# Kernel optimization log

Hardware: AMD Instinct MI355X
Metric: run time of the kernel (lower is better)

## Reference

```python
import jax, jax.numpy as jnp
import numpy as np

L, B = 128, 4
N_D, N_E, N_PROJ, DEPTH = 1024, 256, 256, 4
N_V = 128000
CUTOFFS = (10000, 20000, 40000, 60000, 100000)  # hard-coded in Model.__init__
N_CLUSTERS = len(CUTOFFS)
HIGHWAY_BIAS = -3.0  # args.bias, added to forget-gate bias
EMB_SCALE = float(np.sqrt(N_D))


def setup_inputs() -> dict:
    key = jax.random.key(0)
    ks = jax.random.split(key, 10)
    s = 0.02
    return {
        "x": jax.random.randint(ks[0], (L, B), 0, N_V),
        "y": jax.random.randint(ks[1], (L, B), 0, N_V),
        "hidden": jnp.zeros((DEPTH, B, N_D), jnp.float32),
        "emb_weight": jax.random.normal(ks[2], (N_V, N_E), jnp.float32) * s,
        "emb_proj": jax.random.normal(ks[3], (N_D, N_E), jnp.float32) * s,
        "out_bias": jnp.zeros((N_V,), jnp.float32),
        "cluster_weight": jax.random.normal(ks[4], (N_CLUSTERS, N_E), jnp.float32) * s,
        "cluster_bias": jnp.zeros((N_CLUSTERS,), jnp.float32),
        "Wp": jax.random.normal(ks[5], (DEPTH, N_D, N_PROJ), jnp.float32) * s,
        "Wq": jax.random.normal(ks[6], (DEPTH, N_PROJ, 3 * N_D), jnp.float32) * s,
        "wc": jax.random.normal(ks[7], (DEPTH, 2 * N_D), jnp.float32) * s,
        "b": jnp.zeros((DEPTH, 2 * N_D), jnp.float32),
    }


def _sru_layer(h, c0, Wp_l, Wq_l, wc_l, b_l):
    # Projected linear: [L,B,n_d] @ [n_d,n_proj] @ [n_proj,3*n_d]
    u = ((h @ Wp_l) @ Wq_l).reshape(L, B, 3, N_D)
    u0, u1, u2 = u[..., 0, :], u[..., 1, :], u[..., 2, :]
    vf, vr = wc_l[:N_D], wc_l[N_D:]
    bf = b_l[:N_D] + HIGHWAY_BIAS
    br = b_l[N_D:]

    def step(c, uu):
        u0t, u1t, u2t, xt = uu
        f = jax.nn.sigmoid(u1t + vf * c + bf)
        r = jax.nn.sigmoid(u2t + vr * c + br)
        c_new = f * c + (1.0 - f) * u0t
        h_t = r * c_new + (1.0 - r) * xt  # highway connection (rescale off)
        return c_new, h_t

    c_last, hs = jax.lax.scan(step, c0, (u0, u1, u2, h))
    return hs, c_last


def reference(x, y, hidden, emb_weight, emb_proj, out_bias, cluster_weight,
              cluster_bias, Wp, Wq, wc, b):
    # Adaptive embedding (div_val=1: single table + projection), scaled by sqrt(n_d)
    h = (emb_weight[x] @ emb_proj.T) * EMB_SCALE  # [L,B,n_d]
    c_finals = []
    for l in range(DEPTH):
        h, cl = _sru_layer(h, hidden[l], Wp[l], Wq[l], wc[l], b[l])
        c_finals.append(cl)
    hid_out = jnp.stack(c_finals)  # [depth,B,n_d]

    out = h.reshape(-1, N_D)       # [N, n_d]
    proj_h = out @ emb_proj        # tied out_proj: [N, n_e]
    c0 = CUTOFFS[0]

    # Head: first cutoff tokens + cluster logits
    head_w = jnp.concatenate([emb_weight[:c0], cluster_weight], axis=0)
    head_b = jnp.concatenate([out_bias[:c0], cluster_bias], axis=0)
    head_lp = jax.nn.log_softmax(proj_h @ head_w.T + head_b, axis=-1)  # [N, c0+5]

    # Tail logits over all tail tokens; per-cluster logsumexp via static slices
    tail_logits = proj_h @ emb_weight[c0:].T + out_bias[c0:]  # [N, N_V-c0]
    bounds = list(CUTOFFS) + [N_V]
    lses = jnp.stack(
        [jax.scipy.special.logsumexp(tail_logits[:, bounds[i] - c0:bounds[i + 1] - c0], axis=-1)
         for i in range(N_CLUSTERS)], axis=-1)  # [N, 5]

    yf = y.reshape(-1)
    cluster = jnp.zeros_like(yf)
    for cu in CUTOFFS:
        cluster = cluster + (yf >= cu).astype(yf.dtype)  # 0=head, 1..5=tails
    n_idx = jnp.arange(yf.shape[0])
    logit_y = jnp.sum(proj_h * emb_weight[yf], axis=-1) + out_bias[yf]
    tci = jnp.clip(cluster - 1, 0, N_CLUSTERS - 1)
    tail_lp_y = logit_y - lses[n_idx, tci]
    head_tok_lp = head_lp[n_idx, jnp.minimum(yf, c0 - 1)]
    cluster_lp = head_lp[n_idx, c0 + tci]
    lp = jnp.where(cluster == 0, head_tok_lp, cluster_lp + tail_lp_y)
    loss = (-lp).reshape(L, B)
    return loss, hid_out
```

## Files before the change

kernel.cpp:

```cpp
#include <hip/hip_runtime.h>
#include <hip/hip_bf16.h>
#include <math.h>

#define LSEQ 128
#define BB 4
#define NTOK 512
#define ND 1024
#define NE 256
#define NPROJ 256
#define DEPTH 4
#define NV 128000
#define NC 5
#define C0 10000
#define NHEADROWS 128005
#define NROWS_PAD 128128

typedef unsigned short u16;
typedef __bf16 bf16x8 __attribute__((ext_vector_type(8)));
typedef float  f32x4  __attribute__((ext_vector_type(4)));
typedef u16    u16x8  __attribute__((ext_vector_type(8)));
typedef u16    u16x4  __attribute__((ext_vector_type(4)));

__device__ inline u16 f2bf_rne(float f) {
  unsigned int u = __float_as_uint(f);
  u += 0x7FFFu + ((u >> 16) & 1u);
  return (u16)(u >> 16);
}
__device__ inline unsigned int f2hilo_pk(float v) {
  unsigned int u = __float_as_uint(v);
  u16 h = (u16)(u >> 16);
  u16 l = f2bf_rne(v - __uint_as_float(u & 0xFFFF0000u));
  return (unsigned int)h | ((unsigned int)l << 16);
}

__global__ __launch_bounds__(256) void conv_emb(
    const float* __restrict__ emb, const float* __restrict__ cw,
    u16* __restrict__ Wb) {
  const long NCH = (long)NHEADROWS * NE / 8;
  const long EMBN = (long)NV * NE;
  for (long i = (long)blockIdx.x * 256 + threadIdx.x; i < NCH; i += (long)gridDim.x * 256) {
    long e = i * 8;
    const float* src = (e < EMBN) ? emb + e : cw + (e - EMBN);
    float4 a = *reinterpret_cast<const float4*>(src);
    float4 b = *reinterpret_cast<const float4*>(src + 4);
    u16x8 o;
    o[0] = f2bf_rne(a.x); o[1] = f2bf_rne(a.y); o[2] = f2bf_rne(a.z); o[3] = f2bf_rne(a.w);
    o[4] = f2bf_rne(b.x); o[5] = f2bf_rne(b.y); o[6] = f2bf_rne(b.z); o[7] = f2bf_rne(b.w);
    *reinterpret_cast<u16x8*>(Wb + e) = o;
  }
}

__global__ __launch_bounds__(256) void conv_hilo(
    const float* __restrict__ src, u16* __restrict__ dh, u16* __restrict__ dl, long n4) {
  for (long i = (long)blockIdx.x * 256 + threadIdx.x; i < n4; i += (long)gridDim.x * 256) {
    float4 a = *reinterpret_cast<const float4*>(src + i * 4);
    unsigned int p0 = f2hilo_pk(a.x), p1 = f2hilo_pk(a.y);
    unsigned int p2 = f2hilo_pk(a.z), p3 = f2hilo_pk(a.w);
    u16x4 h, l;
    h[0] = (u16)p0; l[0] = (u16)(p0 >> 16);
    h[1] = (u16)p1; l[1] = (u16)(p1 >> 16);
    h[2] = (u16)p2; l[2] = (u16)(p2 >> 16);
    h[3] = (u16)p3; l[3] = (u16)(p3 >> 16);
    *reinterpret_cast<u16x4*>(dh + i * 4) = h;
    *reinterpret_cast<u16x4*>(dl + i * 4) = l;
  }
}

__global__ __launch_bounds__(256) void tconv(
    const float* __restrict__ src, u16* __restrict__ dh, u16* __restrict__ dl,
    int K, int N, long sStride, long dStride) {
  __shared__ float t[32][33];
  const int mat = blockIdx.z;
  src += (long)mat * sStride; dh += (long)mat * dStride; dl += (long)mat * dStride;
  const int k0 = blockIdx.y * 32, n0 = blockIdx.x * 32;
  const int lr = threadIdx.x & 31, tr = threadIdx.x >> 5;
#pragma unroll
  for (int i = 0; i < 4; ++i)
    t[tr + i * 8][lr] = src[(size_t)(k0 + tr + i * 8) * N + n0 + lr];
  __syncthreads();
#pragma unroll
  for (int i = 0; i < 4; ++i) {
    int nl = tr + i * 8;
    unsigned int pk = f2hilo_pk(t[lr][nl]);
    size_t o = (size_t)(n0 + nl) * K + k0 + lr;
    dh[o] = (u16)pk; dl[o] = (u16)(pk >> 16);
  }
}

__global__ __launch_bounds__(256) void gather_hilo(
    const int* __restrict__ x, const float* __restrict__ emb,
    u16* __restrict__ Eh, u16* __restrict__ El) {
  int n = blockIdx.x, e = threadIdx.x;
  float v = emb[(size_t)x[n] * NE + e] * 32.0f;
  unsigned int pk = f2hilo_pk(v);
  Eh[(size_t)n * NE + e] = (u16)pk; El[(size_t)n * NE + e] = (u16)(pk >> 16);
}

#define GP 72
template<bool WF32, bool WHILO, bool WRNE>
__global__ __launch_bounds__(256) void gemm3(
    const u16* __restrict__ Ah, const u16* __restrict__ Al,
    const u16* __restrict__ Bh, const u16* __restrict__ Bl,
    float* __restrict__ C, u16* __restrict__ Ch, u16* __restrict__ Cl,
    u16* __restrict__ Cr, int M, int N, int K) {
  __shared__ u16 ash[64][GP], asl[64][GP], bsh[64][GP], bsl[64][GP];
  const int tid = threadIdx.x, lane = tid & 63, w = tid >> 6;
  const int wm = w >> 1, wn = w & 1, lrow = lane & 15, lkg = lane >> 4;
  const int m0 = blockIdx.y * 64, n0 = blockIdx.x * 64;
  f32x4 acc[2][2] = {};
  for (int ks = 0; ks < K; ks += 64) {
#pragma unroll
    for (int i = 0; i < 2; ++i) {
      int idx = tid + 256 * i, r = idx >> 3, c8 = (idx & 7) * 8;
      *reinterpret_cast<u16x8*>(&ash[r][c8]) = *reinterpret_cast<const u16x8*>(Ah + (size_t)(m0 + r) * K + ks + c8);
      *reinterpret_cast<u16x8*>(&asl[r][c8]) = *reinterpret_cast<const u16x8*>(Al + (size_t)(m0 + r) * K + ks + c8);
      *reinterpret_cast<u16x8*>(&bsh[r][c8]) = *reinterpret_cast<const u16x8*>(Bh + (size_t)(n0 + r) * K + ks + c8);
      *reinterpret_cast<u16x8*>(&bsl[r][c8]) = *reinterpret_cast<const u16x8*>(Bl + (size_t)(n0 + r) * K + ks + c8);
    }
    __syncthreads();
#pragma unroll
    for (int k2 = 0; k2 < 2; ++k2) {
      bf16x8 ah[2], al[2], bh[2], bl[2];
#pragma unroll
      for (int mi = 0; mi < 2; ++mi) {
        ah[mi] = *reinterpret_cast<const bf16x8*>(&ash[wm * 32 + mi * 16 + lrow][k2 * 32 + lkg * 8]);
        al[mi] = *reinterpret_cast<const bf16x8*>(&asl[wm * 32 + mi * 16 + lrow][k2 * 32 + lkg * 8]);
      }
#pragma unroll
      for (int ni = 0; ni < 2; ++ni) {
        bh[ni] = *reinterpret_cast<const bf16x8*>(&bsh[wn * 32 + ni * 16 + lrow][k2 * 32 + lkg * 8]);
        bl[ni] = *reinterpret_cast<const bf16x8*>(&bsl[wn * 32 + ni * 16 + lrow][k2 * 32 + lkg * 8]);
      }
#pragma unroll
      for (int mi = 0; mi < 2; ++mi)
#pragma unroll
        for (int ni = 0; ni < 2; ++ni) {
          acc[mi][ni] = __builtin_amdgcn_mfma_f32_16x16x32_bf16(ah[mi], bh[ni], acc[mi][ni], 0, 0, 0);
          acc[mi][ni] = __builtin_amdgcn_mfma_f32_16x16x32_bf16(ah[mi], bl[ni], acc[mi][ni], 0, 0, 0);
          acc[mi][ni] = __builtin_amdgcn_mfma_f32_16x16x32_bf16(al[mi], bh[ni], acc[mi][ni], 0, 0, 0);
        }
    }
    __syncthreads();
  }
#pragma unroll
  for (int mi = 0; mi < 2; ++mi)
#pragma unroll
    for (int ni = 0; ni < 2; ++ni)
#pragma unroll
      for (int j = 0; j < 4; ++j) {
        int row = m0 + wm * 32 + mi * 16 + lkg * 4 + j;
        int col = n0 + wn * 32 + ni * 16 + lrow;
        float v = acc[mi][ni][j];
        size_t o = (size_t)row * N + col;
        if (WF32) C[o] = v;
        if (WHILO) { unsigned int pk = f2hilo_pk(v); Ch[o] = (u16)pk; Cl[o] = (u16)(pk >> 16); }
        if (WRNE) Cr[o] = f2bf_rne(v);
      }
}

__global__ __launch_bounds__(256) void sru_scan(
    const float* __restrict__ u, const float* __restrict__ h_in,
    const float* __restrict__ hidden, const float* __restrict__ wcv,
    const float* __restrict__ bvec, float* __restrict__ h_out,
    u16* __restrict__ hOh, u16* __restrict__ hOl,
    float* __restrict__ out, int layer) {
  int idx = blockIdx.x * 256 + threadIdx.x;
  int b = idx >> 10, d = idx & 1023;
  float c = hidden[layer * (BB * ND) + idx];
  float vf = wcv[layer * 2 * ND + d];
  float vr = wcv[layer * 2 * ND + ND + d];
  float bf = bvec[layer * 2 * ND + d] + (-3.0f);
  float br = bvec[layer * 2 * ND + ND + d];
  for (int t0 = 0; t0 < LSEQ; t0 += 4) {
    float u0[4], u1[4], u2[4], xt[4];
#pragma unroll
    for (int q = 0; q < 4; ++q) {
      size_t row = (size_t)(t0 + q) * BB + b;
      u0[q] = u[row * (3 * ND) + d];
      u1[q] = u[row * (3 * ND) + ND + d];
      u2[q] = u[row * (3 * ND) + 2 * ND + d];
      xt[q] = h_in[row * ND + d];
    }
#pragma unroll
    for (int q = 0; q < 4; ++q) {
      float f = 1.f / (1.f + __expf(-(u1[q] + vf * c + bf)));
      float r = 1.f / (1.f + __expf(-(u2[q] + vr * c + br)));
      c = f * c + (1.f - f) * u0[q];
      float h = r * c + (1.f - r) * xt[q];
      size_t row = (size_t)(t0 + q) * BB + b;
      h_out[row * ND + d] = h;
      unsigned int pk = f2hilo_pk(h);
      hOh[row * ND + d] = (u16)pk; hOl[row * ND + d] = (u16)(pk >> 16);
    }
  }
  out[NTOK + layer * (BB * ND) + idx] = c;
}

__device__ inline int seg_of(int v) {
  if (v < 10000)  return 5;
  if (v < 20000)  return 0;
  if (v < 40000)  return 1;
  if (v < 60000)  return 2;
  if (v < 100000) return 3;
  if (v < 128000) return 4;
  if (v < 128005) return 5;
  return -1;
}

__global__ __launch_bounds__(256) void head_tail(
    const u16* __restrict__ Wb, const float* __restrict__ ob,
    const float* __restrict__ cb, const u16* __restrict__ phb,
    float* __restrict__ accum) {
  __shared__ u16 As[128][GP];
  __shared__ u16 Bs[128][GP];
  __shared__ float red[128][6];
  const int tid = threadIdx.x, lane = tid & 63, w = tid >> 6;
  const int wr = w >> 1, wcq = w & 1, lrow = lane & 15, lkg = lane >> 4;

  const int nwg = gridDim.x;
  const int orig = blockIdx.x;
  const int xcd = orig & 7, i8 = orig >> 3;
  const int q = nwg >> 3, r8 = nwg & 7;
  const int swz = (xcd < r8 ? xcd * (q + 1) : r8 * (q + 1) + (xcd - r8) * q) + i8;
  const int v0 = (swz >> 2) * 128;
  const int n0 = (swz & 3) * 128;

  f32x4 acc[4][4] = {};
  for (int ks = 0; ks < NE; ks += 64) {
#pragma unroll
    for (int i = 0; i < 4; ++i) {
      int idx = tid + 256 * i, rr = idx >> 3, c8 = (idx & 7) * 8;
      *reinterpret_cast<u16x8*>(&As[rr][c8]) =
          *reinterpret_cast<const u16x8*>(Wb + (size_t)(v0 + rr) * NE + ks + c8);
    }
#pragma unroll
    for (int i = 0; i < 4; ++i) {
      int idx = tid + 256 * i, rr = idx >> 3, c8 = (idx & 7) * 8;
      *reinterpret_cast<u16x8*>(&Bs[rr][c8]) =
          *reinterpret_cast<const u16x8*>(phb + (size_t)(n0 + rr) * NE + ks + c8);
    }
    __syncthreads();
#pragma unroll
    for (int k2 = 0; k2 < 2; ++k2) {
      bf16x8 av[4], bv[4];
#pragma unroll
      for (int mi = 0; mi < 4; ++mi)
        av[mi] = *reinterpret_cast<const bf16x8*>(&As[wr * 64 + mi * 16 + lrow][k2 * 32 + lkg * 8]);
#pragma unroll
      for (int ni = 0; ni < 4; ++ni)
        bv[ni] = *reinterpret_cast<const bf16x8*>(&Bs[wcq * 64 + ni * 16 + lrow][k2 * 32 + lkg * 8]);
#pragma unroll
      for (int mi = 0; mi < 4; ++mi)
#pragma unroll
        for (int ni = 0; ni < 4; ++ni)
          acc[mi][ni] = __builtin_amdgcn_mfma_f32_16x16x32_bf16(av[mi], bv[ni], acc[mi][ni], 0, 0, 0);
    }
    __syncthreads();
  }

  for (int i = tid; i < 128 * 6; i += 256) red[i / 6][i % 6] = 0.f;
  __syncthreads();
#pragma unroll
  for (int ni = 0; ni < 4; ++ni) {
    int tok = wcq * 64 + ni * 16 + lrow;
    float s[6] = {0.f, 0.f, 0.f, 0.f, 0.f, 0.f};
#pragma unroll
    for (int mi = 0; mi < 4; ++mi) {
#pragma unroll
      for (int j = 0; j < 4; ++j) {
        int v = v0 + wr * 64 + mi * 16 + lkg * 4 + j;
        int seg = seg_of(v);
        if (seg >= 0) {
          float bias = (v < NV) ? ob[v] : cb[v - NV];
          s[seg] += expf(acc[mi][ni][j] + bias);
        }
      }
    }
#pragma unroll
    for (int sg = 0; sg < 6; ++sg)
      if (s[sg] != 0.f) atomicAdd(&red[tok][sg], s[sg]);
  }
  __syncthreads();
  for (int i = tid; i < 128 * 6; i += 256) {
    float s = red[i / 6][i % 6];
    if (s != 0.f) atomicAdd(&accum[(size_t)(n0 + i / 6) * 6 + (i % 6)], s);
  }
}

__global__ __launch_bounds__(64) void loss_kernel(
    const float* __restrict__ ph, const float* __restrict__ emb,
    const float* __restrict__ cw, const float* __restrict__ ob,
    const float* __restrict__ cb, const int* __restrict__ y,
    const float* __restrict__ accum, float* __restrict__ out) {
  int n = blockIdx.x, lane = threadIdx.x;
  int yv = y[n];
  int cluster = (yv >= 10000) + (yv >= 20000) + (yv >= 40000) + (yv >= 60000) + (yv >= 100000);
  int tci = min(max(cluster - 1, 0), NC - 1);
  int hy = min(yv, C0 - 1);
  float d1 = 0.f, d2 = 0.f, d3 = 0.f;
  for (int k = lane; k < NE; k += 64) {
    float p = ph[(size_t)n * NE + k];
    d1 += p * emb[(size_t)yv * NE + k];
    d2 += p * emb[(size_t)hy * NE + k];
    d3 += p * cw[(size_t)tci * NE + k];
  }
#pragma unroll
  for (int off = 32; off > 0; off >>= 1) {
    d1 += __shfl_down(d1, off);
    d2 += __shfl_down(d2, off);
    d3 += __shfl_down(d3, off);
  }
  if (lane == 0) {
    float logit_y = d1 + ob[yv];
    float head_tok = d2 + ob[hy];
    float clus = d3 + cb[tci];
    float head_lse = logf(accum[(size_t)n * 6 + 5]);
    float lp;
    if (cluster == 0) lp = head_tok - head_lse;
    else lp = (clus - head_lse) + (logit_y - logf(accum[(size_t)n * 6 + tci]));
    out[n] = -lp;
  }
}

extern "C" void kernel_launch(void* const* d_in, const int* in_sizes, int n_in,
                              void* d_out, int out_size, void* d_ws, size_t ws_size,
                              hipStream_t stream) {
  const int*   x      = (const int*)d_in[0];
  const int*   y      = (const int*)d_in[1];
  const float* hidden = (const float*)d_in[2];
  const float* emb    = (const float*)d_in[3];
  const float* eproj  = (const float*)d_in[4];
  const float* obias  = (const float*)d_in[5];
  const float* cwp    = (const float*)d_in[6];
  const float* cbp    = (const float*)d_in[7];
  const float* Wp     = (const float*)d_in[8];
  const float* Wq     = (const float*)d_in[9];
  const float* wcv    = (const float*)d_in[10];
  const float* bvec   = (const float*)d_in[11];
  float* out = (float*)d_out;

  char* p = (char*)d_ws;
  auto alloc = [&](size_t bytes) { char* r = p; p += (bytes + 255) & ~(size_t)255; return r; };
  u16*   WbB   = (u16*)alloc((size_t)NROWS_PAD * NE * 2);
  u16*   epH   = (u16*)alloc((size_t)ND * NE * 2);
  u16*   epL   = (u16*)alloc((size_t)ND * NE * 2);
  u16*   epTH  = (u16*)alloc((size_t)NE * ND * 2);
  u16*   epTL  = (u16*)alloc((size_t)NE * ND * 2);
  u16*   WpTH  = (u16*)alloc((size_t)DEPTH * NPROJ * ND * 2);
  u16*   WpTL  = (u16*)alloc((size_t)DEPTH * NPROJ * ND * 2);
  u16*   WqTH  = (u16*)alloc((size_t)DEPTH * 3 * ND * NPROJ * 2);
  u16*   WqTL  = (u16*)alloc((size_t)DEPTH * 3 * ND * NPROJ * 2);
  u16*   ExH   = (u16*)alloc((size_t)NTOK * NE * 2);
  u16*   ExL   = (u16*)alloc((size_t)NTOK * NE * 2);
  float* h0    = (float*)alloc((size_t)NTOK * ND * 4);
  float* h1    = (float*)alloc((size_t)NTOK * ND * 4);
  u16*   h0H   = (u16*)alloc((size_t)NTOK * ND * 2);
  u16*   h0L   = (u16*)alloc((size_t)NTOK * ND * 2);
  u16*   h1H   = (u16*)alloc((size_t)NTOK * ND * 2);
  u16*   h1L   = (u16*)alloc((size_t)NTOK * ND * 2);
  u16*   PH    = (u16*)alloc((size_t)NTOK * NPROJ * 2);
  u16*   PL    = (u16*)alloc((size_t)NTOK * NPROJ * 2);
  float* U     = (float*)alloc((size_t)NTOK * 3 * ND * 4);
  float* projh = (float*)alloc((size_t)NTOK * NE * 4);
  u16*   phb   = (u16*)alloc((size_t)NTOK * NE * 2);
  float* accum = (float*)alloc((size_t)NTOK * 6 * 4);

  (void)hipMemsetAsync(accum, 0, (size_t)NTOK * 6 * 4, stream);

  conv_hilo<<<256, 256, 0, stream>>>(eproj, epH, epL, (long)ND * NE / 4);
  tconv<<<dim3(NE / 32, ND / 32, 1), 256, 0, stream>>>(eproj, epTH, epTL, ND, NE, 0, 0);
  tconv<<<dim3(NPROJ / 32, ND / 32, DEPTH), 256, 0, stream>>>(
      Wp, WpTH, WpTL, ND, NPROJ, (long)ND * NPROJ, (long)ND * NPROJ);
  tconv<<<dim3(3 * ND / 32, NPROJ / 32, DEPTH), 256, 0, stream>>>(
      Wq, WqTH, WqTL, NPROJ, 3 * ND, (long)NPROJ * 3 * ND, (long)NPROJ * 3 * ND);
  gather_hilo<<<NTOK, NE, 0, stream>>>(x, emb, ExH, ExL);

  gemm3<true, true, false><<<dim3(ND / 64, NTOK / 64), 256, 0, stream>>>(
      ExH, ExL, epH, epL, h0, h0H, h0L, nullptr, NTOK, ND, NE);

  float* hcF = h0; u16* hcH = h0H; u16* hcL = h0L;
  float* hnF = h1; u16* hnH = h1H; u16* hnL = h1L;
  for (int l = 0; l < DEPTH; ++l) {
    gemm3<false, true, false><<<dim3(NPROJ / 64, NTOK / 64), 256, 0, stream>>>(
        hcH, hcL, WpTH + (size_t)l * NPROJ * ND, WpTL + (size_t)l * NPROJ * ND,
        nullptr, PH, PL, nullptr, NTOK, NPROJ, ND);
    gemm3<true, false, false><<<dim3(3 * ND / 64, NTOK / 64), 256, 0, stream>>>(
        PH, PL, WqTH + (size_t)l * 3 * ND * NPROJ, WqTL + (size_t)l * 3 * ND * NPROJ,
        U, nullptr, nullptr, nullptr, NTOK, 3 * ND, NPROJ);
    sru_scan<<<16, 256, 0, stream>>>(U, hcF, hidden, wcv, bvec, hnF, hnH, hnL, out, l);
    { float* t = hcF; hcF = hnF; hnF = t; }
    { u16* t = hcH; hcH = hnH; hnH = t; }
    { u16* t = hcL; hcL = hnL; hnL = t; }
  }

  gemm3<true, false, true><<<dim3(NE / 64, NTOK / 64), 256, 0, stream>>>(
      hcH, hcL, epTH, epTL, projh, nullptr, nullptr, phb, NTOK, NE, ND);

  conv_emb<<<2048, 256, 0, stream>>>(emb, cwp, WbB);

  head_tail<<<dim3((NTOK / 128) * (NROWS_PAD / 128)), 256, 0, stream>>>(
      WbB, obias, cbp, phb, accum);

  loss_kernel<<<NTOK, 64, 0, stream>>>(projh, emb, cwp, obias, cbp, y, accum, out);
}
```

Before: 648.2 us.

## Double-buffer head GEMM with direct-to-LDS loads, swizzle, and prefetch SRU inputs

The head/tail logsumexp GEMM now stages tiles with global_load_lds into double-buffered, XOR-swizzled shared memory, so the next K slice loads while MFMAs run. LDS bank conflicts are reduced without the padding. Its epilogue hoists the segment lookup per 16-row group, uses __expf, and issues one atomic per group instead of six-way branching. The SRU scan software-pipelines its global loads by prefetching the next 4 timesteps. These trade a simpler structure for more registers and LDS, plus fast-math exp precision.

```diff
diff --git a/kernel.cpp b/kernel.cpp
--- a/kernel.cpp
+++ b/kernel.cpp
@@ -31,6 +31,12 @@
   u16 h = (u16)(u >> 16);
   u16 l = f2bf_rne(v - __uint_as_float(u & 0xFFFF0000u));
   return (unsigned int)h | ((unsigned int)l << 16);
+}
+
+__device__ __forceinline__ void gld16(const u16* g, u16* l) {
+  __builtin_amdgcn_global_load_lds(
+      (const __attribute__((address_space(1))) void*)g,
+      (__attribute__((address_space(3))) void*)l, 16, 0, 0);
 }
 
 __global__ __launch_bounds__(256) void conv_emb(
@@ -158,6 +164,35 @@
       }
 }
 
+__device__ __forceinline__ void sru_load(
+    const float* __restrict__ u, const float* __restrict__ h_in, int t0, int b, int d,
+    float (&u0)[4], float (&u1)[4], float (&u2)[4], float (&xt)[4]) {
+#pragma unroll
+  for (int q = 0; q < 4; ++q) {
+    size_t row = (size_t)(t0 + q) * BB + b;
+    u0[q] = u[row * (3 * ND) + d];
+    u1[q] = u[row * (3 * ND) + ND + d];
+    u2[q] = u[row * (3 * ND) + 2 * ND + d];
+    xt[q] = h_in[row * ND + d];
+  }
+}
+__device__ __forceinline__ void sru_step(
+    int t0, int b, int d, float& c, float vf, float vr, float bf, float br,
+    const float (&u0)[4], const float (&u1)[4], const float (&u2)[4], const float (&xt)[4],
+    float* __restrict__ h_out, u16* __restrict__ hOh, u16* __restrict__ hOl) {
+#pragma unroll
+  for (int q = 0; q < 4; ++q) {
+    float f = 1.f / (1.f + __expf(-(u1[q] + vf * c + bf)));
+    float r = 1.f / (1.f + __expf(-(u2[q] + vr * c + br)));
+    c = f * c + (1.f - f) * u0[q];
+    float h = r * c + (1.f - r) * xt[q];
+    size_t row = (size_t)(t0 + q) * BB + b;
+    h_out[row * ND + d] = h;
+    unsigned int pk = f2hilo_pk(h);
+    hOh[row * ND + d] = (u16)pk; hOl[row * ND + d] = (u16)(pk >> 16);
+  }
+}
+
 __global__ __launch_bounds__(256) void sru_scan(
     const float* __restrict__ u, const float* __restrict__ h_in,
     const float* __restrict__ hidden, const float* __restrict__ wcv,
@@ -171,27 +206,13 @@
   float vr = wcv[layer * 2 * ND + ND + d];
   float bf = bvec[layer * 2 * ND + d] + (-3.0f);
   float br = bvec[layer * 2 * ND + ND + d];
-  for (int t0 = 0; t0 < LSEQ; t0 += 4) {
-    float u0[4], u1[4], u2[4], xt[4];
-#pragma unroll
-    for (int q = 0; q < 4; ++q) {
-      size_t row = (size_t)(t0 + q) * BB + b;
-      u0[q] = u[row * (3 * ND) + d];
-      u1[q] = u[row * (3 * ND) + ND + d];
-      u2[q] = u[row * (3 * ND) + 2 * ND + d];
-      xt[q] = h_in[row * ND + d];
-    }
-#pragma unroll
-    for (int q = 0; q < 4; ++q) {
-      float f = 1.f / (1.f + __expf(-(u1[q] + vf * c + bf)));
-      float r = 1.f / (1.f + __expf(-(u2[q] + vr * c + br)));
-      c = f * c + (1.f - f) * u0[q];
-      float h = r * c + (1.f - r) * xt[q];
-      size_t row = (size_t)(t0 + q) * BB + b;
-      h_out[row * ND + d] = h;
-      unsigned int pk = f2hilo_pk(h);
-      hOh[row * ND + d] = (u16)pk; hOl[row * ND + d] = (u16)(pk >> 16);
-    }
+  float A0[4], A1[4], A2[4], A3[4], B0[4], B1[4], B2[4], B3[4];
+  sru_load(u, h_in, 0, b, d, A0, A1, A2, A3);
+  for (int t0 = 0; t0 < LSEQ; t0 += 8) {
+    sru_load(u, h_in, t0 + 4, b, d, B0, B1, B2, B3);
+    sru_step(t0, b, d, c, vf, vr, bf, br, A0, A1, A2, A3, h_out, hOh, hOl);
+    if (t0 + 8 < LSEQ) sru_load(u, h_in, t0 + 8, b, d, A0, A1, A2, A3);
+    sru_step(t0 + 4, b, d, c, vf, vr, bf, br, B0, B1, B2, B3, h_out, hOh, hOl);
   }
   out[NTOK + layer * (BB * ND) + idx] = c;
 }
@@ -211,8 +232,8 @@
     const u16* __restrict__ Wb, const float* __restrict__ ob,
     const float* __restrict__ cb, const u16* __restrict__ phb,
     float* __restrict__ accum) {
-  __shared__ u16 As[128][GP];
-  __shared__ u16 Bs[128][GP];
+  __shared__ u16 As[2][128][64];
+  __shared__ u16 Bs[2][128][64];
   __shared__ float red[128][6];
   const int tid = threadIdx.x, lane = tid & 63, w = tid >> 6;
   const int wr = w >> 1, wcq = w & 1, lrow = lane & 15, lkg = lane >> 4;
@@ -220,35 +241,54 @@
   const int nwg = gridDim.x;
   const int orig = blockIdx.x;
   const int xcd = orig & 7, i8 = orig >> 3;
-  const int q = nwg >> 3, r8 = nwg & 7;
-  const int swz = (xcd < r8 ? xcd * (q + 1) : r8 * (q + 1) + (xcd - r8) * q) + i8;
+  const int q8 = nwg >> 3, r8 = nwg & 7;
+  const int swz = (xcd < r8 ? xcd * (q8 + 1) : r8 * (q8 + 1) + (xcd - r8) * q8) + i8;
   const int v0 = (swz >> 2) * 128;
   const int n0 = (swz & 3) * 128;
 
+  int srow[4], scol[4];
+#pragma unroll
+  for (int i = 0; i < 4; ++i) {
+    int cch = tid + 256 * i;
+    srow[i] = cch >> 3;
+    scol[i] = ((cch & 7) ^ ((cch >> 3) & 7)) * 8;
+  }
+  const u16* gA = Wb  + (size_t)v0 * NE;
+  const u16* gB = phb + (size_t)n0 * NE;
+  const int dchunk = w * 64;
+
   f32x4 acc[4][4] = {};
-  for (int ks = 0; ks < NE; ks += 64) {
+
+  auto stage = [&](int buf, int ks) {
 #pragma unroll
     for (int i = 0; i < 4; ++i) {
-      int idx = tid + 256 * i, rr = idx >> 3, c8 = (idx & 7) * 8;
-      *reinterpret_cast<u16x8*>(&As[rr][c8]) =
-          *reinterpret_cast<const u16x8*>(Wb + (size_t)(v0 + rr) * NE + ks + c8);
-    }
-#pragma unroll
-    for (int i = 0; i < 4; ++i) {
-      int idx = tid + 256 * i, rr = idx >> 3, c8 = (idx & 7) * 8;
-      *reinterpret_cast<u16x8*>(&Bs[rr][c8]) =
-          *reinterpret_cast<const u16x8*>(phb + (size_t)(n0 + rr) * NE + ks + c8);
-    }
-    __syncthreads();
+      gld16(gA + (size_t)srow[i] * NE + ks + scol[i],
+            &As[buf][0][0] + (size_t)(dchunk + 256 * i) * 8);
+      gld16(gB + (size_t)srow[i] * NE + ks + scol[i],
+            &Bs[buf][0][0] + (size_t)(dchunk + 256 * i) * 8);
+    }
+  };
+
+  stage(0, 0);
+  __syncthreads();
+#pragma unroll
+  for (int t = 0; t < 4; ++t) {
+    if (t < 3) stage((t + 1) & 1, (t + 1) * 64);
+    const int buf = t & 1;
 #pragma unroll
     for (int k2 = 0; k2 < 2; ++k2) {
       bf16x8 av[4], bv[4];
-#pragma unroll
-      for (int mi = 0; mi < 4; ++mi)
-        av[mi] = *reinterpret_cast<const bf16x8*>(&As[wr * 64 + mi * 16 + lrow][k2 * 32 + lkg * 8]);
-#pragma unroll
-      for (int ni = 0; ni < 4; ++ni)
-        bv[ni] = *reinterpret_cast<const bf16x8*>(&Bs[wcq * 64 + ni * 16 + lrow][k2 * 32 + lkg * 8]);
+      const int qc = k2 * 4 + lkg;
+#pragma unroll
+      for (int mi = 0; mi < 4; ++mi) {
+        int R = wr * 64 + mi * 16 + lrow;
+        av[mi] = *reinterpret_cast<const bf16x8*>(&As[buf][R][(qc ^ (R & 7)) * 8]);
+      }
+#pragma unroll
+      for (int ni = 0; ni < 4; ++ni) {
+        int R = wcq * 64 + ni * 16 + lrow;
+        bv[ni] = *reinterpret_cast<const bf16x8*>(&Bs[buf][R][(qc ^ (R & 7)) * 8]);
+      }
 #pragma unroll
       for (int mi = 0; mi < 4; ++mi)
 #pragma unroll
@@ -258,31 +298,35 @@
     __syncthreads();
   }
 
-  for (int i = tid; i < 128 * 6; i += 256) red[i / 6][i % 6] = 0.f;
+  for (int i = tid; i < 128 * 6; i += 256) (&red[0][0])[i] = 0.f;
   __syncthreads();
 #pragma unroll
-  for (int ni = 0; ni < 4; ++ni) {
-    int tok = wcq * 64 + ni * 16 + lrow;
-    float s[6] = {0.f, 0.f, 0.f, 0.f, 0.f, 0.f};
-#pragma unroll
-    for (int mi = 0; mi < 4; ++mi) {
+  for (int mi = 0; mi < 4; ++mi) {
+    const int vbase = v0 + wr * 64 + mi * 16;
+    const int seg = seg_of(vbase);
+    if (seg < 0) continue;
+    float bj[4]; bool ok[4];
+#pragma unroll
+    for (int j = 0; j < 4; ++j) {
+      int v = vbase + lkg * 4 + j;
+      ok[j] = (v < NHEADROWS);
+      bj[j] = ok[j] ? ((v < NV) ? ob[v] : cb[v - NV]) : 0.f;
+    }
+#pragma unroll
+    for (int ni = 0; ni < 4; ++ni) {
+      int tok = wcq * 64 + ni * 16 + lrow;
+      float s = 0.f;
 #pragma unroll
       for (int j = 0; j < 4; ++j) {
-        int v = v0 + wr * 64 + mi * 16 + lkg * 4 + j;
-        int seg = seg_of(v);
-        if (seg >= 0) {
-          float bias = (v < NV) ? ob[v] : cb[v - NV];
-          s[seg] += expf(acc[mi][ni][j] + bias);
-        }
-      }
-    }
-#pragma unroll
-    for (int sg = 0; sg < 6; ++sg)
-      if (s[sg] != 0.f) atomicAdd(&red[tok][sg], s[sg]);
+        float e = __expf(acc[mi][ni][j] + bj[j]);
+        s += ok[j] ? e : 0.f;
+      }
+      atomicAdd(&red[tok][seg], s);
+    }
   }
   __syncthreads();
   for (int i = tid; i < 128 * 6; i += 256) {
-    float s = red[i / 6][i % 6];
+    float s = (&red[0][0])[i];
     if (s != 0.f) atomicAdd(&accum[(size_t)(n0 + i / 6) * 6 + (i % 6)], s);
   }
 }
```

Result: faster. 622.3 us (-4.0%).
